# Kernel optimization log

Hardware: AMD Instinct MI355X
Metric: run time of the kernel (lower is better)

## Reference

```python
import jax, jax.numpy as jnp
import numpy as np

NUM_HEADS = 8
CHUNK = 64


def _retention(q, k, v):
    # q, k: (B, H, L, DK); v: (B, H, L, DV). Chunked linear retention with
    # per-head exponential decay gamma_h = 1 - 2^(-5-h) (RetNet convention).
    B, Hn, L, DK = q.shape
    DV = v.shape[-1]
    C = CHUNK
    N = L // C
    dt = q.dtype
    gamma = (1.0 - jnp.exp2(-5.0 - jnp.arange(Hn, dtype=jnp.float32))).astype(dt)  # (H,)
    q = q * (DK ** -0.5)
    idx = jnp.arange(C)
    diff = idx[:, None] - idx[None, :]
    # intra-chunk causal decay mask D[h,i,j] = gamma_h^(i-j) for i>=j else 0
    D = jnp.where(diff >= 0, gamma[:, None, None] ** diff, 0.0).astype(dt)      # (H,C,C)
    decay_q = (gamma[:, None] ** (idx[None, :] + 1)).astype(dt)                 # (H,C)
    decay_k = (gamma[:, None] ** (C - 1 - idx[None, :])).astype(dt)             # (H,C)
    decay_s = (gamma ** C).astype(dt)                                           # (H,)

    def to_chunks(x):
        return jnp.moveaxis(x.reshape(B, Hn, N, C, -1), 2, 0)  # (N,B,H,C,d)

    qs, ks, vs = map(to_chunks, (q, k, v))

    def step(S, x):
        qc, kc, vc = x  # (B,H,C,dk) / (B,H,C,dv)
        attn = jnp.einsum('bhid,bhjd->bhij', qc, kc) * D
        o_intra = jnp.einsum('bhij,bhje->bhie', attn, vc)
        o_inter = jnp.einsum('bhid,bhde->bhie', qc * decay_q[None, :, :, None], S)
        S_new = decay_s[None, :, None, None] * S + jnp.einsum(
            'bhjd,bhje->bhde', kc * decay_k[None, :, :, None], vc)
        return S_new, o_intra + o_inter

    S0 = jnp.zeros((B, Hn, DK, DV), dt)
    _, o = jax.lax.scan(step, S0, (qs, ks, vs))  # (N,B,H,C,DV)
    return jnp.moveaxis(o, 0, 2).reshape(B, Hn, L, DV)


def _xavier(key, fan_in, fan_out, gain=2 ** (-2.5)):
    limit = gain * np.sqrt(6.0 / (fan_in + fan_out))
    return jax.random.uniform(key, (fan_in, fan_out), jnp.float32, -limit, limit)


def setup_inputs() -> dict:
    key = jax.random.key(0)
    k0, k1, k2, k3, k4 = jax.random.split(key, 5)
    B, L, D = 2, 4096, 1024
    return {
        'hidden_states': jax.random.normal(k0, (B, L, D), jnp.float32),
        'rel_pos': jnp.zeros((1,), jnp.float32),  # unused by the module's forward
        'Wq': _xavier(k1, D, D),
        'Wk': _xavier(k2, D, D),
        'Wv': _xavier(k3, D, D),
        'Wo': _xavier(k4, D, D),
    }


def reference(hidden_states, rel_pos, Wq, Wk, Wv, Wo):
    B, L, Dm = hidden_states.shape
    Hd = Dm // NUM_HEADS
    q = (hidden_states @ Wq).reshape(B, L, NUM_HEADS, Hd).transpose(0, 2, 1, 3)
    k = (hidden_states @ Wk).reshape(B, L, NUM_HEADS, Hd).transpose(0, 2, 1, 3)
    v = (hidden_states @ Wv).reshape(B, L, NUM_HEADS, Hd).transpose(0, 2, 1, 3)
    o = _retention(q, k, v)  # (B,H,L,Hd)
    o = o.transpose(0, 2, 1, 3).reshape(B, L, Dm)
    return o @ Wo
```

## Files before the change

### kernel.cpp

```cpp
#include <hip/hip_runtime.h>
#include <hip/hip_bf16.h>

typedef __bf16 bf16;
typedef __bf16 bf16x8 __attribute__((ext_vector_type(8)));
typedef float f32x4 __attribute__((ext_vector_type(4)));

#define MFMA16(a, b, c) __builtin_amdgcn_mfma_f32_16x16x32_bf16((a), (b), (c), 0, 0, 0)


__device__ __forceinline__ void g2l16(const bf16* g, bf16* l) {
  __builtin_amdgcn_global_load_lds(
      (const __attribute__((address_space(1))) void*)g,
      (__attribute__((address_space(3))) void*)l, 16, 0, 0);
}

__global__ __launch_bounds__(256) void cvt_bf16(const float* __restrict__ X,
                                                bf16* __restrict__ Y) {
  const size_t i = ((size_t)blockIdx.x * 256 + threadIdx.x) * 8;
  float4 a = *(const float4*)&X[i];
  float4 b = *(const float4*)&X[i + 4];
  union { bf16 h[8]; uint4 u; } p;
  p.h[0] = (bf16)a.x; p.h[1] = (bf16)a.y; p.h[2] = (bf16)a.z; p.h[3] = (bf16)a.w;
  p.h[4] = (bf16)b.x; p.h[5] = (bf16)b.y; p.h[6] = (bf16)b.z; p.h[7] = (bf16)b.w;
  *(uint4*)&Y[i] = p.u;
}

__global__ __launch_bounds__(256) void transpose_w(
    const float* __restrict__ Wq, const float* __restrict__ Wk,
    const float* __restrict__ Wv, const float* __restrict__ Wo,
    bf16* __restrict__ Wt) {
  __shared__ bf16 t[64 * 72];
  const float* src = (blockIdx.z == 0) ? Wq : (blockIdx.z == 1) ? Wk
                     : (blockIdx.z == 2) ? Wv : Wo;
  bf16* dst = Wt + (size_t)blockIdx.z * 1024 * 1024;
  const int k0 = blockIdx.x * 64, n0 = blockIdx.y * 64;
  const int tid = threadIdx.x;
#pragma unroll
  for (int s = 0; s < 4; ++s) {
    int u = tid + s * 256;
    int r = u >> 4, c4 = (u & 15) * 4;
    float4 f = *(const float4*)&src[(size_t)(k0 + r) * 1024 + n0 + c4];
    t[r * 72 + c4 + 0] = (bf16)f.x;
    t[r * 72 + c4 + 1] = (bf16)f.y;
    t[r * 72 + c4 + 2] = (bf16)f.z;
    t[r * 72 + c4 + 3] = (bf16)f.w;
  }
  __syncthreads();
#pragma unroll
  for (int s = 0; s < 2; ++s) {
    int u = tid + s * 256;
    int r = u >> 3, cc = u & 7;
    union { bf16 h[8]; uint4 u4; } pk;
#pragma unroll
    for (int j = 0; j < 8; ++j) pk.h[j] = t[(cc * 8 + j) * 72 + r];
    *(uint4*)&dst[(size_t)(n0 + r) * 1024 + k0 + cc * 8] = pk.u4;
  }
}

template <typename TC, int QKV>
__global__ __launch_bounds__(256) void gemm_lds(
    const bf16* __restrict__ A, const bf16* __restrict__ Bt,
    TC* __restrict__ C, float alpha) {
  __shared__ bf16 lA[128 * 64];
  __shared__ bf16 lB[128 * 64];
  const int m0 = blockIdx.x * 128, n0 = blockIdx.y * 128;
  if (QKV) {
    Bt += (size_t)blockIdx.z * 1024 * 1024;
    C += (size_t)blockIdx.z * 8192 * 1024;
    if (blockIdx.z != 0) alpha = 1.0f;
  }
  const int tid = threadIdx.x;
  const int w = tid >> 6, lane = tid & 63, lr = lane & 15, quad = lane >> 4;
  const int wm = w >> 1, wn = w & 1;

  const int srow = w * 32 + (lane >> 3);
  const int clog = (lane & 7) ^ ((lane >> 3) & 7);
  const bf16* gA = A + (size_t)(m0 + srow) * 1024 + clog * 8;
  const bf16* gB = Bt + (size_t)(n0 + srow) * 1024 + clog * 8;

  f32x4 acc[4][4] = {};

  for (int it = 0; it < 16; ++it) {
    const int k0 = it * 64;
#pragma unroll
    for (int is = 0; is < 4; ++is) {
      g2l16(gA + (size_t)is * 8 * 1024 + k0, &lA[(w * 32 + is * 8) * 64]);
      g2l16(gB + (size_t)is * 8 * 1024 + k0, &lB[(w * 32 + is * 8) * 64]);
    }
    __syncthreads();
#pragma unroll
    for (int kk = 0; kk < 2; ++kk) {
      bf16x8 af[4], bfv[4];
#pragma unroll
      for (int i = 0; i < 4; ++i) {
        const int m = wm * 64 + i * 16 + lr;
        af[i] = *(bf16x8*)&lA[m * 64 + (((kk * 4 + quad) ^ (lr & 7)) * 8)];
      }
#pragma unroll
      for (int j = 0; j < 4; ++j) {
        const int n = wn * 64 + j * 16 + lr;
        bfv[j] = *(bf16x8*)&lB[n * 64 + (((kk * 4 + quad) ^ (lr & 7)) * 8)];
      }
#pragma unroll
      for (int i = 0; i < 4; ++i)
#pragma unroll
        for (int j = 0; j < 4; ++j)
          acc[i][j] = MFMA16(af[i], bfv[j], acc[i][j]);
    }
    __syncthreads();
  }
#pragma unroll
  for (int i = 0; i < 4; ++i) {
#pragma unroll
    for (int j = 0; j < 4; ++j) {
      const int row = m0 + wm * 64 + i * 16 + quad * 4;
      const int col = n0 + wn * 64 + j * 16 + lr;
#pragma unroll
      for (int r = 0; r < 4; ++r)
        C[(size_t)(row + r) * 1024 + col] = (TC)(acc[i][j][r] * alpha);
    }
  }
}

__global__ __launch_bounds__(256) void chunk_kv(
    const bf16* __restrict__ kb, const bf16* __restrict__ vb,
    bf16* __restrict__ Tb) {
  __shared__ bf16 lK[128 * 72];
  __shared__ bf16 lV[128 * 72];
  const int g = blockIdx.x;
  const int bh = g >> 6, n = g & 63, b = bh >> 3, h = bh & 7;
  const float log2g = log2f(1.0f - exp2f(-5.0f - (float)h));
  const int tid = threadIdx.x;
  const size_t rowbase = (size_t)(b * 4096 + n * 64) * 1024 + h * 128;
  const bf16* kc = kb + rowbase;
  const bf16* vc = vb + rowbase;
#pragma unroll
  for (int s = 0; s < 4; ++s) {
    int u = tid + s * 256;
    int c = u >> 4, d0 = (u & 15) * 8;
    union { uint4 u4; bf16 h8[8]; } kv, vv;
    kv.u4 = *(const uint4*)&kc[(size_t)c * 1024 + d0];
    vv.u4 = *(const uint4*)&vc[(size_t)c * 1024 + d0];
    const float dec = exp2f((float)(63 - c) * log2g);
#pragma unroll
    for (int j = 0; j < 8; ++j) {
      lK[(d0 + j) * 72 + c] = (bf16)((float)kv.h8[j] * dec);
      lV[(d0 + j) * 72 + c] = vv.h8[j];
    }
  }
  __syncthreads();
  const int w = tid >> 6, lane = tid & 63, lr = lane & 15, quad = lane >> 4;
  const int wm = w >> 1, wn = w & 1;
  f32x4 acc[4][4] = {};
#pragma unroll
  for (int kk = 0; kk < 2; ++kk) {
    bf16x8 af[4], bv[4];
#pragma unroll
    for (int i = 0; i < 4; ++i)
      af[i] = *(bf16x8*)&lK[(wm * 64 + i * 16 + lr) * 72 + kk * 32 + quad * 8];
#pragma unroll
    for (int j = 0; j < 4; ++j)
      bv[j] = *(bf16x8*)&lV[(wn * 64 + j * 16 + lr) * 72 + kk * 32 + quad * 8];
#pragma unroll
    for (int i = 0; i < 4; ++i)
#pragma unroll
      for (int j = 0; j < 4; ++j)
        acc[i][j] = MFMA16(af[i], bv[j], acc[i][j]);
  }
  bf16* tchunk = Tb + (size_t)g * 16384;
#pragma unroll
  for (int i = 0; i < 4; ++i) {
#pragma unroll
    for (int j = 0; j < 4; ++j) {
      const int dk = wm * 64 + i * 16 + quad * 4;
      const int dv = wn * 64 + j * 16 + lr;
      union { bf16 h4[4]; uint2 u2; } pk;
#pragma unroll
      for (int r = 0; r < 4; ++r) pk.h4[r] = (bf16)acc[i][j][r];
      *(uint2*)&tchunk[(size_t)dv * 128 + dk] = pk.u2;
    }
  }
}

__global__ __launch_bounds__(256) void scan_state(bf16* __restrict__ Tb) {
  const int blk = blockIdx.x;
  const int bh = blk >> 6, seg = blk & 63, h = bh & 7;
  const float gs = exp2f(64.0f * log2f(1.0f - exp2f(-5.0f - (float)h)));
  const size_t base = (size_t)bh * 64 * 16384 + (size_t)seg * 256 + threadIdx.x;
  float S = 0.0f;
#pragma unroll 8
  for (int n = 0; n < 64; ++n) {
    const size_t a = base + (size_t)n * 16384;
    const float t = (float)Tb[a];
    Tb[a] = (bf16)S;
    S = gs * S + t;
  }
}

__global__ __launch_bounds__(256) void chunk_out(
    const bf16* __restrict__ qb, const bf16* __restrict__ kb,
    const bf16* __restrict__ vb, const bf16* __restrict__ Sp,
    bf16* __restrict__ ob) {
  __shared__ bf16 lQ[64 * 136];
  __shared__ bf16 lK[64 * 136];
  __shared__ bf16 lVt[128 * 72];
  __shared__ bf16 lP[64 * 72];
  const int g = blockIdx.x;
  const int bh = g >> 6, n = g & 63, b = bh >> 3, h = bh & 7;
  const float log2g = log2f(1.0f - exp2f(-5.0f - (float)h));
  const int tid = threadIdx.x;
  const size_t rowbase = (size_t)(b * 4096 + n * 64) * 1024 + h * 128;
  const bf16* qc = qb + rowbase;
  const bf16* kc = kb + rowbase;
  const bf16* vc = vb + rowbase;
#pragma unroll
  for (int s = 0; s < 4; ++s) {
    int u = tid + s * 256;
    int c = u >> 4, d0 = (u & 15) * 8;
    *(uint4*)&lQ[c * 136 + d0] = *(const uint4*)&qc[(size_t)c * 1024 + d0];
    *(uint4*)&lK[c * 136 + d0] = *(const uint4*)&kc[(size_t)c * 1024 + d0];
    union { uint4 u4; bf16 h8[8]; } vv;
    vv.u4 = *(const uint4*)&vc[(size_t)c * 1024 + d0];
#pragma unroll
    for (int j = 0; j < 8; ++j) lVt[(d0 + j) * 72 + c] = vv.h8[j];
  }
  __syncthreads();
  const int w = tid >> 6, lane = tid & 63, lr = lane & 15, quad = lane >> 4;

  f32x4 p[4] = {};
#pragma unroll
  for (int kk = 0; kk < 4; ++kk) {
    bf16x8 bfrag = *(bf16x8*)&lK[(w * 16 + lr) * 136 + kk * 32 + quad * 8];
#pragma unroll
    for (int i = 0; i < 4; ++i) {
      bf16x8 afrag = *(bf16x8*)&lQ[(i * 16 + lr) * 136 + kk * 32 + quad * 8];
      p[i] = MFMA16(afrag, bfrag, p[i]);
    }
  }
#pragma unroll
  for (int i = 0; i < 4; ++i) {
#pragma unroll
    for (int r = 0; r < 4; ++r) {
      const int row = i * 16 + quad * 4 + r;
      const int col = w * 16 + lr;
      const int diff = row - col;
      const float val =
          (diff >= 0) ? p[i][r] * exp2f((float)diff * log2g) : 0.0f;
      lP[row * 72 + col] = (bf16)val;
    }
  }
  __syncthreads();

  f32x4 oacc[4][2] = {};
#pragma unroll
  for (int j = 0; j < 2; ++j) {
    const int dvt = w * 32 + j * 16;
#pragma unroll
    for (int kk = 0; kk < 2; ++kk) {
      bf16x8 bfrag = *(bf16x8*)&lVt[(dvt + lr) * 72 + kk * 32 + quad * 8];
#pragma unroll
      for (int i = 0; i < 4; ++i) {
        bf16x8 afrag = *(bf16x8*)&lP[(i * 16 + lr) * 72 + kk * 32 + quad * 8];
        oacc[i][j] = MFMA16(afrag, bfrag, oacc[i][j]);
      }
    }
  }

  const bf16* sp = Sp + (size_t)g * 16384;
#pragma unroll
  for (int kk = 0; kk < 4; ++kk) {
    bf16x8 aN[4];
#pragma unroll
    for (int i = 0; i < 4; ++i) {
      bf16x8 a0 = *(bf16x8*)&lQ[(i * 16 + lr) * 136 + kk * 32 + quad * 8];
      const float dq = exp2f((float)(i * 16 + lr + 1) * log2g);
#pragma unroll
      for (int e = 0; e < 8; ++e) a0[e] = (bf16)((float)a0[e] * dq);
      aN[i] = a0;
    }
#pragma unroll
    for (int j = 0; j < 2; ++j) {
      bf16x8 bfrag =
          *(const bf16x8*)&sp[(size_t)(w * 32 + j * 16 + lr) * 128 + kk * 32 + quad * 8];
#pragma unroll
      for (int i = 0; i < 4; ++i) oacc[i][j] = MFMA16(aN[i], bfrag, oacc[i][j]);
    }
  }

  bf16* oc = ob + rowbase;
#pragma unroll
  for (int i = 0; i < 4; ++i)
#pragma unroll
    for (int j = 0; j < 2; ++j)
#pragma unroll
      for (int r = 0; r < 4; ++r) {
        const int row = i * 16 + quad * 4 + r;
        const int col = w * 32 + j * 16 + lr;
        oc[(size_t)row * 1024 + col] = (bf16)oacc[i][j][r];
      }
}

extern "C" void kernel_launch(void* const* d_in, const int* in_sizes, int n_in,
                              void* d_out, int out_size, void* d_ws,
                              size_t ws_size, hipStream_t stream) {
  const float* X  = (const float*)d_in[0];
  const float* Wq = (const float*)d_in[2];
  const float* Wk = (const float*)d_in[3];
  const float* Wv = (const float*)d_in[4];
  const float* Wo = (const float*)d_in[5];

  char* ws = (char*)d_ws;
  const size_t SZ_QKV = (size_t)8192 * 1024 * sizeof(bf16);
  bf16* qb = (bf16*)(ws);
  bf16* ob = (bf16*)(ws + 3 * SZ_QKV);
  bf16* Tb = (bf16*)(ws + 4 * SZ_QKV);
  bf16* Wt = (bf16*)(ws + 6 * SZ_QKV);
  bf16* Xb = (bf16*)(ws + 6 * SZ_QKV + (size_t)4 * 1024 * 1024 * sizeof(bf16));
  bf16* kb = qb + (size_t)8192 * 1024;
  bf16* vb = kb + (size_t)8192 * 1024;

  cvt_bf16<<<4096, 256, 0, stream>>>(X, Xb);
  transpose_w<<<dim3(16, 16, 4), 256, 0, stream>>>(Wq, Wk, Wv, Wo, Wt);

  const float qscale = 0.08838834764831845f;
  gemm_lds<bf16, 1><<<dim3(64, 8, 3), 256, 0, stream>>>(Xb, Wt, qb, qscale);

  chunk_kv<<<1024, 256, 0, stream>>>(kb, vb, Tb);
  scan_state<<<1024, 256, 0, stream>>>(Tb);
  chunk_out<<<1024, 256, 0, stream>>>(qb, kb, vb, Tb, ob);

  gemm_lds<float, 0><<<dim3(64, 8), 256, 0, stream>>>(
      ob, Wt + (size_t)3 * 1024 * 1024, (float*)d_out, 1.0f);
}
```

Baseline: 230.9 us.

## Replace GEMM with triple-buffered 512-thread pipelined kernel using 256x128 tiles

Rewrites the LDS GEMM into a 3-stage software pipeline that prefetches tiles two k-steps ahead with global_load_lds, split around the two MFMA halves with explicit vmcnt waits and barriers. Tiles grow to 256x128 with 8 waves, and the QKV GEMM becomes a single 2D grid that picks its output slab from the column index. MFMA sections are wrapped in s_setprio. The goal is to hide global-load latency and drop one of the two per-iteration syncthreads, at the cost of more LDS use (144KB) and hand-tuned wait counts that must stay correct.

Result: slower. 239.3 us (+3.6%).

```diff
diff --git a/kernel.cpp b/kernel.cpp
--- a/kernel.cpp
+++ b/kernel.cpp
@@ -58,63 +58,94 @@
 }
 
 template <typename TC, int QKV>
-__global__ __launch_bounds__(256) void gemm_lds(
+__global__ __launch_bounds__(512, 2) void gemm_pipe(
     const bf16* __restrict__ A, const bf16* __restrict__ Bt,
     TC* __restrict__ C, float alpha) {
-  __shared__ bf16 lA[128 * 64];
-  __shared__ bf16 lB[128 * 64];
-  const int m0 = blockIdx.x * 128, n0 = blockIdx.y * 128;
+  __shared__ bf16 lds[3 * 24576];
+  const int m0 = blockIdx.x * 256;
+  const int n0g = blockIdx.y * 128;
+  int ncol0 = n0g;
   if (QKV) {
-    Bt += (size_t)blockIdx.z * 1024 * 1024;
-    C += (size_t)blockIdx.z * 8192 * 1024;
-    if (blockIdx.z != 0) alpha = 1.0f;
+    const int z = n0g >> 10;
+    C += (size_t)z * (8192 * 1024);
+    if (z != 0) alpha = 1.0f;
+    ncol0 = n0g & 1023;
   }
   const int tid = threadIdx.x;
   const int w = tid >> 6, lane = tid & 63, lr = lane & 15, quad = lane >> 4;
   const int wm = w >> 1, wn = w & 1;
-
-  const int srow = w * 32 + (lane >> 3);
-  const int clog = (lane & 7) ^ ((lane >> 3) & 7);
-  const bf16* gA = A + (size_t)(m0 + srow) * 1024 + clog * 8;
-  const bf16* gB = Bt + (size_t)(n0 + srow) * 1024 + clog * 8;
+  const int srow8 = lane >> 3;
+  const int clog = (lane & 7) ^ srow8;
+
+  const bf16* gA = A + (size_t)(m0 + w * 8 + srow8) * 1024 + clog * 8;
+  const bf16* gB = Bt + (size_t)(n0g + w * 8 + srow8) * 1024 + clog * 8;
+  const int lrow = w * 8 * 64;
+
+#define STAGE_A(tt, bi, is)                                       \
+  g2l16(gA + (size_t)(is) * 64 * 1024 + (tt) * 64,                \
+        &lds[(bi) * 24576 + (is) * 4096 + lrow])
+#define STAGE_B(tt, bi, is)                                       \
+  g2l16(gB + (size_t)(is) * 64 * 1024 + (tt) * 64,                \
+        &lds[(bi) * 24576 + 16384 + (is) * 4096 + lrow])
 
   f32x4 acc[4][4] = {};
 
-  for (int it = 0; it < 16; ++it) {
-    const int k0 = it * 64;
-#pragma unroll
-    for (int is = 0; is < 4; ++is) {
-      g2l16(gA + (size_t)is * 8 * 1024 + k0, &lA[(w * 32 + is * 8) * 64]);
-      g2l16(gB + (size_t)is * 8 * 1024 + k0, &lB[(w * 32 + is * 8) * 64]);
-    }
-    __syncthreads();
-#pragma unroll
-    for (int kk = 0; kk < 2; ++kk) {
-      bf16x8 af[4], bfv[4];
-#pragma unroll
-      for (int i = 0; i < 4; ++i) {
-        const int m = wm * 64 + i * 16 + lr;
-        af[i] = *(bf16x8*)&lA[m * 64 + (((kk * 4 + quad) ^ (lr & 7)) * 8)];
-      }
-#pragma unroll
-      for (int j = 0; j < 4; ++j) {
-        const int n = wn * 64 + j * 16 + lr;
-        bfv[j] = *(bf16x8*)&lB[n * 64 + (((kk * 4 + quad) ^ (lr & 7)) * 8)];
-      }
-#pragma unroll
-      for (int i = 0; i < 4; ++i)
-#pragma unroll
-        for (int j = 0; j < 4; ++j)
-          acc[i][j] = MFMA16(af[i], bfv[j], acc[i][j]);
-    }
-    __syncthreads();
-  }
+  STAGE_A(0, 0, 0); STAGE_A(0, 0, 1); STAGE_A(0, 0, 2); STAGE_A(0, 0, 3);
+  STAGE_B(0, 0, 0); STAGE_B(0, 0, 1);
+  STAGE_A(1, 1, 0); STAGE_A(1, 1, 1); STAGE_A(1, 1, 2); STAGE_A(1, 1, 3);
+  STAGE_B(1, 1, 0); STAGE_B(1, 1, 1);
+  asm volatile("s_waitcnt vmcnt(6)" ::: "memory");
+  asm volatile("s_barrier" ::: "memory");
+
+  const int sw0 = (quad ^ (lr & 7)) * 8;
+  const int sw1 = ((4 + quad) ^ (lr & 7)) * 8;
+  const int arow = (wm * 64 + lr) * 64;
+  const int brow = (wn * 64 + lr) * 64;
+
+  int cb = 0, sb = 2;
+#pragma unroll 1
+  for (int t = 0; t < 16; ++t) {
+    const bf16* LA = &lds[cb * 24576];
+    const bf16* LB = LA + 16384;
+    if (t < 14) { STAGE_A(t + 2, sb, 0); STAGE_A(t + 2, sb, 1); STAGE_A(t + 2, sb, 2); }
+    bf16x8 af[4], bv[4];
+#pragma unroll
+    for (int i = 0; i < 4; ++i) af[i] = *(const bf16x8*)&LA[arow + i * 1024 + sw0];
+#pragma unroll
+    for (int j = 0; j < 4; ++j) bv[j] = *(const bf16x8*)&LB[brow + j * 1024 + sw0];
+    __builtin_amdgcn_s_setprio(1);
+#pragma unroll
+    for (int i = 0; i < 4; ++i)
+#pragma unroll
+      for (int j = 0; j < 4; ++j) acc[i][j] = MFMA16(af[i], bv[j], acc[i][j]);
+    __builtin_amdgcn_s_setprio(0);
+    asm volatile("s_barrier" ::: "memory");
+    if (t < 14) { STAGE_A(t + 2, sb, 3); STAGE_B(t + 2, sb, 0); STAGE_B(t + 2, sb, 1); }
+#pragma unroll
+    for (int i = 0; i < 4; ++i) af[i] = *(const bf16x8*)&LA[arow + i * 1024 + sw1];
+#pragma unroll
+    for (int j = 0; j < 4; ++j) bv[j] = *(const bf16x8*)&LB[brow + j * 1024 + sw1];
+    __builtin_amdgcn_s_setprio(1);
+#pragma unroll
+    for (int i = 0; i < 4; ++i)
+#pragma unroll
+      for (int j = 0; j < 4; ++j) acc[i][j] = MFMA16(af[i], bv[j], acc[i][j]);
+    __builtin_amdgcn_s_setprio(0);
+    if (t < 14) asm volatile("s_waitcnt vmcnt(6)" ::: "memory");
+    else        asm volatile("s_waitcnt vmcnt(0)" ::: "memory");
+    asm volatile("s_barrier" ::: "memory");
+    cb = (cb == 2) ? 0 : cb + 1;
+    sb = (sb == 2) ? 0 : sb + 1;
+  }
+#undef STAGE_A
+#undef STAGE_B
+
 #pragma unroll
   for (int i = 0; i < 4; ++i) {
 #pragma unroll
     for (int j = 0; j < 4; ++j) {
       const int row = m0 + wm * 64 + i * 16 + quad * 4;
-      const int col = n0 + wn * 64 + j * 16 + lr;
+      const int col = ncol0 + wn * 64 + j * 16 + lr;
 #pragma unroll
       for (int r = 0; r < 4; ++r)
         C[(size_t)(row + r) * 1024 + col] = (TC)(acc[i][j][r] * alpha);
@@ -323,12 +354,12 @@
   transpose_w<<<dim3(16, 16, 4), 256, 0, stream>>>(Wq, Wk, Wv, Wo, Wt);
 
   const float qscale = 0.08838834764831845f;
-  gemm_lds<bf16, 1><<<dim3(64, 8, 3), 256, 0, stream>>>(Xb, Wt, qb, qscale);
+  gemm_pipe<bf16, 1><<<dim3(32, 24), 512, 0, stream>>>(Xb, Wt, qb, qscale);
 
   chunk_kv<<<1024, 256, 0, stream>>>(kb, vb, Tb);
   scan_state<<<1024, 256, 0, stream>>>(Tb);
   chunk_out<<<1024, 256, 0, stream>>>(qb, kb, vb, Tb, ob);
 
-  gemm_lds<float, 0><<<dim3(64, 8), 256, 0, stream>>>(
+  gemm_pipe<float, 0><<<dim3(32, 8), 512, 0, stream>>>(
       ob, Wt + (size_t)3 * 1024 * 1024, (float*)d_out, 1.0f);
 }
```
